# Performance work log

Hardware: AMD Instinct MI355X
Metric: run time of the kernel (lower is better)

## Reference

```python
import jax, jax.numpy as jnp
import numpy as np

B, N, INP = 16, 1024, 256
HEADS, DIM_HEAD = 8, 32
INNER = HEADS * DIM_HEAD  # 256
OUP = 256
IH = IW = 32  # IH*IW == N


def _relative_index(ih, iw):
    # mirrors the torch __init__ construction (meshgrid indexing='ij')
    coords = np.stack(np.meshgrid(np.arange(ih), np.arange(iw), indexing='ij')).reshape(2, -1)
    rel = coords[:, :, None] - coords[:, None, :]  # [2, N, N]
    rel[0] += ih - 1
    rel[1] += iw - 1
    rel[0] *= 2 * iw - 1
    return rel.sum(0).reshape(-1)  # [N*N]


def setup_inputs() -> dict:
    key = jax.random.key(0)
    kx, kqkv, kout, kbias = jax.random.split(key, 4)
    x = jax.random.normal(kx, (B, N, INP), dtype=jnp.float32)
    w_qkv = jax.random.normal(kqkv, (INP, 3 * INNER), dtype=jnp.float32) * 0.02
    w_out = jax.random.normal(kout, (INNER, OUP), dtype=jnp.float32) * 0.02
    b_out = jnp.zeros((OUP,), dtype=jnp.float32)
    bias_table = jax.random.normal(kbias, ((2 * IH - 1) * (2 * IW - 1), HEADS), dtype=jnp.float32) * 0.02
    relative_index = jnp.asarray(_relative_index(IH, IW), dtype=jnp.int32)
    return {"x": x, "w_qkv": w_qkv, "w_out": w_out, "b_out": b_out,
            "bias_table": bias_table, "relative_index": relative_index}


def reference(x, w_qkv, w_out, b_out, bias_table, relative_index):
    b, n, _ = x.shape
    scale = DIM_HEAD ** (-0.5)
    qkv = x @ w_qkv  # [b, n, 3*inner]
    q, k, v = jnp.split(qkv, 3, axis=-1)
    split_heads = lambda t: t.reshape(b, n, HEADS, DIM_HEAD).transpose(0, 2, 1, 3)  # b h n d
    q, k, v = split_heads(q), split_heads(k), split_heads(v)
    dots = jnp.einsum('bhnd,bhmd->bhnm', q, k) * scale  # [b, h, n, n]
    # gather bias: (n*n, heads) -> (1, heads, n, n), matching '(h w) c -> 1 c h w'
    rel_bias = bias_table[relative_index].reshape(n, n, HEADS).transpose(2, 0, 1)[None]
    attn = jax.nn.softmax(dots + rel_bias, axis=-1)
    out = jnp.einsum('bhnm,bhmd->bhnd', attn, v)
    out = out.transpose(0, 2, 1, 3).reshape(b, n, INNER)  # b n (h d)
    return out @ w_out + b_out
```

## Files before the change

### kernel.cpp

```cpp
#include <hip/hip_runtime.h>
#include <hip/hip_bf16.h>

typedef __bf16 bf16;
typedef bf16 bf16x4 __attribute__((ext_vector_type(4)));
typedef bf16 bf16x8 __attribute__((ext_vector_type(8)));
typedef short s16x4 __attribute__((ext_vector_type(4)));
typedef float f32x4 __attribute__((ext_vector_type(4)));

#define MFMA32(A, B, C) __builtin_amdgcn_mfma_f32_16x16x32_bf16(A, B, C, 0, 0, 0)
#define MFMA16(A, B, C) __builtin_amdgcn_mfma_f32_16x16x16bf16_1k(A, B, C, 0, 0, 0)
#define GL2LDS16(gp, lp)                                                            \
  __builtin_amdgcn_global_load_lds((const __attribute__((address_space(1))) unsigned int*)(gp), \
                                   (__attribute__((address_space(3))) unsigned int*)(lp), 16, 0, 0)

static constexpr float SCALE = 0.17677669529663687f;
static constexpr float LOG2E = 1.4426950408889634f;

__global__ __launch_bounds__(256) void k_prep(const float* __restrict__ x,
                                              const float* __restrict__ wqkv,
                                              const float* __restrict__ wout,
                                              const float* __restrict__ table,
                                              const int* __restrict__ ridx,
                                              bf16* __restrict__ xb, bf16* __restrict__ wtq,
                                              bf16* __restrict__ wto, bf16* __restrict__ rbb) {
  const int tid = threadIdx.x;
  const int blk = blockIdx.x;
  if (blk < 2048) {
    int t = blk * 256 + tid;
    const float4* s = reinterpret_cast<const float4*>(x) + (size_t)t * 2;
    float4 a = s[0], c = s[1];
    bf16x8 o;
    o[0] = (bf16)a.x; o[1] = (bf16)a.y; o[2] = (bf16)a.z; o[3] = (bf16)a.w;
    o[4] = (bf16)c.x; o[5] = (bf16)c.y; o[6] = (bf16)c.z; o[7] = (bf16)c.w;
    reinterpret_cast<bf16x8*>(xb)[t] = o;
  } else if (blk < 3072) {
    int t = (blk - 2048) * 256 + tid;
    if (t < 196608) {
      int n = t >> 8, k = t & 255;
      wtq[t] = (bf16)wqkv[k * 768 + n];
    } else {
      int t2 = t - 196608;
      int n = t2 >> 8, k = t2 & 255;
      wto[t2] = (bf16)wout[k * 256 + n];
    }
  } else {
    const int bb2 = blk - 3072;
    const int qt = bb2 >> 6, kt = bb2 & 63;
    const int r = tid & 3, lane = tid >> 2;
    const int ln = lane & 15, quad = lane >> 4;
    const int qrow = qt * 16 + ln;
    const int key = kt * 16 + quad * 4 + r;
    const int idx = ridx[qrow * 1024 + key];
    const float4* p = reinterpret_cast<const float4*>(table) + idx * 2;
    float4 a = p[0], c = p[1];
    float vals[8] = {a.x, a.y, a.z, a.w, c.x, c.y, c.z, c.w};
    const int base = bb2 * 256 + tid;
#pragma unroll
    for (int h = 0; h < 8; ++h) rbb[h * 1048576 + base] = (bf16)(vals[h] * LOG2E);
  }
}

template <int EPI>
__global__ __launch_bounds__(256) void k_gemm(const bf16* __restrict__ A,
                                              const bf16* __restrict__ Bt,
                                              bf16* __restrict__ q, bf16* __restrict__ kk,
                                              bf16* __restrict__ vt, float* __restrict__ out,
                                              const float* __restrict__ bout) {
  __shared__ __align__(16) bf16 As[2][4096];
  __shared__ __align__(16) bf16 Bs[2][4096];
  const int tid = threadIdx.x;
  const int ln = tid & 15, quad = (tid >> 4) & 3, wv = tid >> 6;
  const int wm = (wv >> 1) * 64, wn = (wv & 1) * 64;
  const int m0 = blockIdx.x * 128, n0 = blockIdx.y * 128;
  const int srow = tid >> 2, scg = (tid & 3) * 8;
  const bf16* ag = A + (size_t)(m0 + srow) * 256 + scg;
  const bf16* bg = Bt + (size_t)(n0 + srow) * 256 + scg;
  f32x4 acc[4][4] = {};

  GL2LDS16(ag, &As[0][tid * 8]);
  GL2LDS16(ag + 64 * 256, &As[0][2048 + tid * 8]);
  GL2LDS16(bg, &Bs[0][tid * 8]);
  GL2LDS16(bg + 64 * 256, &Bs[0][2048 + tid * 8]);

#pragma unroll 2
  for (int kt = 0; kt < 256; kt += 32) {
    const int cur = (kt >> 5) & 1, nxt = cur ^ 1;
    __syncthreads();
    if (kt < 224) {
      GL2LDS16(ag + kt + 32, &As[nxt][tid * 8]);
      GL2LDS16(ag + 64 * 256 + kt + 32, &As[nxt][2048 + tid * 8]);
      GL2LDS16(bg + kt + 32, &Bs[nxt][tid * 8]);
      GL2LDS16(bg + 64 * 256 + kt + 32, &Bs[nxt][2048 + tid * 8]);
    }
    bf16x8 af[4], bfr[4];
#pragma unroll
    for (int i = 0; i < 4; ++i)
      af[i] = *reinterpret_cast<const bf16x8*>(&As[cur][(wm + i * 16 + ln) * 32 + quad * 8]);
#pragma unroll
    for (int i = 0; i < 4; ++i)
      bfr[i] = *reinterpret_cast<const bf16x8*>(&Bs[cur][(wn + i * 16 + ln) * 32 + quad * 8]);
#pragma unroll
    for (int i = 0; i < 4; ++i)
#pragma unroll
      for (int j = 0; j < 4; ++j) acc[i][j] = MFMA32(af[i], bfr[j], acc[i][j]);
  }

  if (EPI == 0) {
    const int colbase = n0 + wn;
    const int seg = colbase >> 8;
    const int cb = colbase & 255;
    const float mul = (seg == 0) ? SCALE * LOG2E : 1.0f;
#pragma unroll
    for (int i = 0; i < 4; ++i) {
      const int gm = m0 + wm + i * 16 + quad * 4;
      const int b = gm >> 10;
#pragma unroll
      for (int j = 0; j < 4; ++j) {
        const int gc = cb + j * 16 + ln;
        const int h = gc >> 5, d = gc & 31;
#pragma unroll
        for (int r = 0; r < 4; ++r) {
          const int nseq = (gm + r) & 1023;
          if (seg == 2) {
            vt[(b * 8 + h) * 32768 + d * 1024 + nseq] = (bf16)acc[i][j][r];
          } else {
            bf16* dst = (seg == 0) ? q : kk;
            dst[(b * 8 + h) * 32768 + nseq * 32 + d] = (bf16)(acc[i][j][r] * mul);
          }
        }
      }
    }
  } else {
#pragma unroll
    for (int j = 0; j < 4; ++j) {
      const int gc = n0 + wn + j * 16 + ln;
      const float bb = bout[gc];
#pragma unroll
      for (int i = 0; i < 4; ++i) {
        const int gm = m0 + wm + i * 16 + quad * 4;
#pragma unroll
        for (int r = 0; r < 4; ++r) out[(size_t)(gm + r) * 256 + gc] = acc[i][j][r] + bb;
      }
    }
  }
}

__global__ __launch_bounds__(256, 6) void k_flash(const bf16* __restrict__ qs,
                                                  const bf16* __restrict__ ks,
                                                  const bf16* __restrict__ vtg,
                                                  const bf16* __restrict__ rbb,
                                                  bf16* __restrict__ ao) {
  __shared__ __align__(16) bf16 Ks[2][2048];
  __shared__ __align__(16) bf16 Vs[2][2048];
  const int tid = threadIdx.x;
  const int lane = tid & 63;
  const int ln = lane & 15, quad = lane >> 4, wv = tid >> 6;
  const int blk = blockIdx.x;
  const int bh = blk & 127;
  const int b = bh >> 3, h = bh & 7;
  const int qtw = (blk >> 7) * 4 + wv;
  const int q0 = qtw * 16;
  const bf16* qb = qs + bh * 32768;
  const bf16* kb = ks + bh * 32768;
  const bf16* vb = vtg + bh * 32768;
  const bf16* bbias = rbb + h * 1048576 + qtw * 16384 + lane * 4;

  const bf16* kg = kb + tid * 8;
  const bf16* vg = vb + (tid & 31) * 1024 + (tid >> 5) * 8;

  const bf16x8 qfrag = *reinterpret_cast<const bf16x8*>(&qb[(q0 + ln) * 32 + quad * 8]);

  f32x4 acc0 = {0.f, 0.f, 0.f, 0.f}, acc1 = {0.f, 0.f, 0.f, 0.f};
  float lsum = 0.f;

  bf16x4 cbf[2][4];
#pragma unroll
  for (int nt = 0; nt < 4; ++nt) cbf[0][nt] = *reinterpret_cast<const bf16x4*>(&bbias[nt * 256]);
  GL2LDS16(kg, &Ks[0][tid * 8]);
  GL2LDS16(vg, &Vs[0][tid * 8]);

#pragma unroll 2
  for (int it = 0; it < 16; ++it) {
    const int cur = it & 1, nxt = cur ^ 1;
    const int k0 = it * 64;
    __syncthreads();
    if (it < 15) {
      GL2LDS16(kg + (k0 + 64) * 32, &Ks[nxt][tid * 8]);
      GL2LDS16(vg + k0 + 64, &Vs[nxt][tid * 8]);
#pragma unroll
      for (int nt = 0; nt < 4; ++nt)
        cbf[nxt][nt] = *reinterpret_cast<const bf16x4*>(&bbias[((it + 1) * 4 + nt) * 256]);
    }
    bf16x8 kf[4];
#pragma unroll
    for (int nt = 0; nt < 4; ++nt)
      kf[nt] = *reinterpret_cast<const bf16x8*>(&Ks[cur][(nt * 16 + ln) * 32 + quad * 8]);
    s16x4 vfa[4], vfc[4];
#pragma unroll
    for (int nt = 0; nt < 4; ++nt) {
      const int base = (2 * nt + (quad >> 1)) * 256 + ln * 8 + (quad & 1) * 4;
      vfa[nt] = *reinterpret_cast<const s16x4*>(&Vs[cur][base]);
      vfc[nt] = *reinterpret_cast<const s16x4*>(&Vs[cur][base + 128]);
    }
    f32x4 s[4];
#pragma unroll
    for (int nt = 0; nt < 4; ++nt) {
      f32x4 c;
#pragma unroll
      for (int e = 0; e < 4; ++e) c[e] = (float)cbf[cur][nt][e];
      s[nt] = MFMA32(kf[nt], qfrag, c);
    }
    s16x4 p[4];
#pragma unroll
    for (int nt = 0; nt < 4; ++nt) {
      bf16x4 t;
#pragma unroll
      for (int e = 0; e < 4; ++e) {
        s[nt][e] = __builtin_amdgcn_exp2f(s[nt][e]);
        t[e] = (bf16)s[nt][e];
      }
      lsum += (s[nt][0] + s[nt][1]) + (s[nt][2] + s[nt][3]);
      p[nt] = __builtin_bit_cast(s16x4, t);
    }
    acc0 = MFMA16(p[0], vfa[0], acc0);
    acc1 = MFMA16(p[0], vfc[0], acc1);
    acc0 = MFMA16(p[1], vfa[1], acc0);
    acc1 = MFMA16(p[1], vfc[1], acc1);
    acc0 = MFMA16(p[2], vfa[2], acc0);
    acc1 = MFMA16(p[2], vfc[2], acc1);
    acc0 = MFMA16(p[3], vfa[3], acc0);
    acc1 = MFMA16(p[3], vfc[3], acc1);
  }
  __syncthreads();

  lsum += __shfl_xor(lsum, 16, 64);
  lsum += __shfl_xor(lsum, 32, 64);

#pragma unroll
  for (int r = 0; r < 4; ++r) {
    const float inv = __builtin_amdgcn_rcpf(__shfl(lsum, quad * 4 + r, 64));
    const int row = q0 + quad * 4 + r;
    bf16* po = &ao[(size_t)(b * 1024 + row) * 256 + h * 32 + ln];
    po[0] = (bf16)(acc0[r] * inv);
    po[16] = (bf16)(acc1[r] * inv);
  }
}

extern "C" void kernel_launch(void* const* d_in, const int* in_sizes, int n_in,
                              void* d_out, int out_size, void* d_ws, size_t ws_size,
                              hipStream_t stream) {
  const float* x = (const float*)d_in[0];
  const float* wqkv = (const float*)d_in[1];
  const float* wout = (const float*)d_in[2];
  const float* bout = (const float*)d_in[3];
  const float* btab = (const float*)d_in[4];
  const int* ridx = (const int*)d_in[5];
  float* out = (float*)d_out;

  char* ws = (char*)d_ws;
  bf16* xb  = (bf16*)(ws + 0);
  bf16* wtq = (bf16*)(ws + 8388608);
  bf16* wto = (bf16*)(ws + 8781824);
  bf16* q   = (bf16*)(ws + 8912896);
  bf16* k   = (bf16*)(ws + 17301504);
  bf16* vt  = (bf16*)(ws + 25690112);
  bf16* rb  = (bf16*)(ws + 34078720);
  bf16* ao  = (bf16*)(ws + 50855936);

  k_prep<<<7168, 256, 0, stream>>>(x, wqkv, wout, btab, ridx, xb, wtq, wto, rb);
  k_gemm<0><<<dim3(128, 6), 256, 0, stream>>>(xb, wtq, q, k, vt, nullptr, nullptr);
  k_flash<<<2048, 256, 0, stream>>>(q, k, vt, rb, ao);
  k_gemm<1><<<dim3(128, 2), 256, 0, stream>>>(ao, wto, nullptr, nullptr, nullptr, out, bout);
}
```

Measured before the change: 155.4 us.

## Process two query tiles per wave in flash kernel and vectorize V-transpose stores

New measurement: 163.3 us. +5.1%, slower.

```diff
diff --git a/kernel.cpp b/kernel.cpp
--- a/kernel.cpp
+++ b/kernel.cpp
@@ -109,22 +109,36 @@
     const int colbase = n0 + wn;
     const int seg = colbase >> 8;
     const int cb = colbase & 255;
-    const float mul = (seg == 0) ? SCALE * LOG2E : 1.0f;
-#pragma unroll
-    for (int i = 0; i < 4; ++i) {
-      const int gm = m0 + wm + i * 16 + quad * 4;
-      const int b = gm >> 10;
-#pragma unroll
-      for (int j = 0; j < 4; ++j) {
-        const int gc = cb + j * 16 + ln;
-        const int h = gc >> 5, d = gc & 31;
-#pragma unroll
-        for (int r = 0; r < 4; ++r) {
-          const int nseq = (gm + r) & 1023;
-          if (seg == 2) {
-            vt[(b * 8 + h) * 32768 + d * 1024 + nseq] = (bf16)acc[i][j][r];
-          } else {
-            bf16* dst = (seg == 0) ? q : kk;
+    if (seg == 2) {
+#pragma unroll
+      for (int i = 0; i < 4; ++i) {
+        const int gm = m0 + wm + i * 16 + quad * 4;
+        const int b = gm >> 10;
+        const int nseq = gm & 1023;
+#pragma unroll
+        for (int j = 0; j < 4; ++j) {
+          const int gc = cb + j * 16 + ln;
+          const int h = gc >> 5, d = gc & 31;
+          bf16x4 v4;
+#pragma unroll
+          for (int r = 0; r < 4; ++r) v4[r] = (bf16)acc[i][j][r];
+          *reinterpret_cast<bf16x4*>(&vt[(b * 8 + h) * 32768 + d * 1024 + nseq]) = v4;
+        }
+      }
+    } else {
+      const float mul = (seg == 0) ? SCALE * LOG2E : 1.0f;
+      bf16* dst = (seg == 0) ? q : kk;
+#pragma unroll
+      for (int i = 0; i < 4; ++i) {
+        const int gm = m0 + wm + i * 16 + quad * 4;
+        const int b = gm >> 10;
+#pragma unroll
+        for (int j = 0; j < 4; ++j) {
+          const int gc = cb + j * 16 + ln;
+          const int h = gc >> 5, d = gc & 31;
+#pragma unroll
+          for (int r = 0; r < 4; ++r) {
+            const int nseq = (gm + r) & 1023;
             dst[(b * 8 + h) * 32768 + nseq * 32 + d] = (bf16)(acc[i][j][r] * mul);
           }
         }
@@ -145,7 +159,7 @@
   }
 }
 
-__global__ __launch_bounds__(256, 6) void k_flash(const bf16* __restrict__ qs,
+__global__ __launch_bounds__(256, 4) void k_flash(const bf16* __restrict__ qs,
                                                   const bf16* __restrict__ ks,
                                                   const bf16* __restrict__ vtg,
                                                   const bf16* __restrict__ rbb,
@@ -158,24 +172,30 @@
   const int blk = blockIdx.x;
   const int bh = blk & 127;
   const int b = bh >> 3, h = bh & 7;
-  const int qtw = (blk >> 7) * 4 + wv;
-  const int q0 = qtw * 16;
+  const int tA = (blk >> 7) * 8 + wv * 2;
+  const int tB = tA + 1;
   const bf16* qb = qs + bh * 32768;
   const bf16* kb = ks + bh * 32768;
   const bf16* vb = vtg + bh * 32768;
-  const bf16* bbias = rbb + h * 1048576 + qtw * 16384 + lane * 4;
+  const bf16* bbA = rbb + h * 1048576 + tA * 16384 + lane * 4;
+  const bf16* bbB = rbb + h * 1048576 + tB * 16384 + lane * 4;
 
   const bf16* kg = kb + tid * 8;
   const bf16* vg = vb + (tid & 31) * 1024 + (tid >> 5) * 8;
 
-  const bf16x8 qfrag = *reinterpret_cast<const bf16x8*>(&qb[(q0 + ln) * 32 + quad * 8]);
-
-  f32x4 acc0 = {0.f, 0.f, 0.f, 0.f}, acc1 = {0.f, 0.f, 0.f, 0.f};
-  float lsum = 0.f;
-
-  bf16x4 cbf[2][4];
-#pragma unroll
-  for (int nt = 0; nt < 4; ++nt) cbf[0][nt] = *reinterpret_cast<const bf16x4*>(&bbias[nt * 256]);
+  const bf16x8 qfA = *reinterpret_cast<const bf16x8*>(&qb[(tA * 16 + ln) * 32 + quad * 8]);
+  const bf16x8 qfB = *reinterpret_cast<const bf16x8*>(&qb[(tB * 16 + ln) * 32 + quad * 8]);
+
+  f32x4 accA0 = {0.f, 0.f, 0.f, 0.f}, accA1 = {0.f, 0.f, 0.f, 0.f};
+  f32x4 accB0 = {0.f, 0.f, 0.f, 0.f}, accB1 = {0.f, 0.f, 0.f, 0.f};
+  float lsA = 0.f, lsB = 0.f;
+
+  bf16x4 cbA[2][4], cbB[2][4];
+#pragma unroll
+  for (int nt = 0; nt < 4; ++nt) {
+    cbA[0][nt] = *reinterpret_cast<const bf16x4*>(&bbA[nt * 256]);
+    cbB[0][nt] = *reinterpret_cast<const bf16x4*>(&bbB[nt * 256]);
+  }
   GL2LDS16(kg, &Ks[0][tid * 8]);
   GL2LDS16(vg, &Vs[0][tid * 8]);
 
@@ -188,8 +208,10 @@
       GL2LDS16(kg + (k0 + 64) * 32, &Ks[nxt][tid * 8]);
       GL2LDS16(vg + k0 + 64, &Vs[nxt][tid * 8]);
 #pragma unroll
-      for (int nt = 0; nt < 4; ++nt)
-        cbf[nxt][nt] = *reinterpret_cast<const bf16x4*>(&bbias[((it + 1) * 4 + nt) * 256]);
+      for (int nt = 0; nt < 4; ++nt) {
+        cbA[nxt][nt] = *reinterpret_cast<const bf16x4*>(&bbA[((it + 1) * 4 + nt) * 256]);
+        cbB[nxt][nt] = *reinterpret_cast<const bf16x4*>(&bbB[((it + 1) * 4 + nt) * 256]);
+      }
     }
     bf16x8 kf[4];
 #pragma unroll
@@ -202,47 +224,86 @@
       vfa[nt] = *reinterpret_cast<const s16x4*>(&Vs[cur][base]);
       vfc[nt] = *reinterpret_cast<const s16x4*>(&Vs[cur][base + 128]);
     }
-    f32x4 s[4];
-#pragma unroll
-    for (int nt = 0; nt < 4; ++nt) {
-      f32x4 c;
-#pragma unroll
-      for (int e = 0; e < 4; ++e) c[e] = (float)cbf[cur][nt][e];
-      s[nt] = MFMA32(kf[nt], qfrag, c);
-    }
-    s16x4 p[4];
-#pragma unroll
-    for (int nt = 0; nt < 4; ++nt) {
-      bf16x4 t;
-#pragma unroll
-      for (int e = 0; e < 4; ++e) {
-        s[nt][e] = __builtin_amdgcn_exp2f(s[nt][e]);
-        t[e] = (bf16)s[nt][e];
-      }
-      lsum += (s[nt][0] + s[nt][1]) + (s[nt][2] + s[nt][3]);
-      p[nt] = __builtin_bit_cast(s16x4, t);
-    }
-    acc0 = MFMA16(p[0], vfa[0], acc0);
-    acc1 = MFMA16(p[0], vfc[0], acc1);
-    acc0 = MFMA16(p[1], vfa[1], acc0);
-    acc1 = MFMA16(p[1], vfc[1], acc1);
-    acc0 = MFMA16(p[2], vfa[2], acc0);
-    acc1 = MFMA16(p[2], vfc[2], acc1);
-    acc0 = MFMA16(p[3], vfa[3], acc0);
-    acc1 = MFMA16(p[3], vfc[3], acc1);
+    {
+      f32x4 s[4];
+#pragma unroll
+      for (int nt = 0; nt < 4; ++nt) {
+        f32x4 c;
+#pragma unroll
+        for (int e = 0; e < 4; ++e) c[e] = (float)cbA[cur][nt][e];
+        s[nt] = MFMA32(kf[nt], qfA, c);
+      }
+      s16x4 p[4];
+#pragma unroll
+      for (int nt = 0; nt < 4; ++nt) {
+        bf16x4 t;
+#pragma unroll
+        for (int e = 0; e < 4; ++e) {
+          s[nt][e] = __builtin_amdgcn_exp2f(s[nt][e]);
+          t[e] = (bf16)s[nt][e];
+        }
+        lsA += (s[nt][0] + s[nt][1]) + (s[nt][2] + s[nt][3]);
+        p[nt] = __builtin_bit_cast(s16x4, t);
+      }
+      accA0 = MFMA16(p[0], vfa[0], accA0);
+      accA1 = MFMA16(p[0], vfc[0], accA1);
+      accA0 = MFMA16(p[1], vfa[1], accA0);
+      accA1 = MFMA16(p[1], vfc[1], accA1);
+      accA0 = MFMA16(p[2], vfa[2], accA0);
+      accA1 = MFMA16(p[2], vfc[2], accA1);
+      accA0 = MFMA16(p[3], vfa[3], accA0);
+      accA1 = MFMA16(p[3], vfc[3], accA1);
+    }
+    {
+      f32x4 s[4];
+#pragma unroll
+      for (int nt = 0; nt < 4; ++nt) {
+        f32x4 c;
+#pragma unroll
+        for (int e = 0; e < 4; ++e) c[e] = (float)cbB[cur][nt][e];
+        s[nt] = MFMA32(kf[nt], qfB, c);
+      }
+      s16x4 p[4];
+#pragma unroll
+      for (int nt = 0; nt < 4; ++nt) {
+        bf16x4 t;
+#pragma unroll
+        for (int e = 0; e < 4; ++e) {
+          s[nt][e] = __builtin_amdgcn_exp2f(s[nt][e]);
+          t[e] = (bf16)s[nt][e];
+        }
+        lsB += (s[nt][0] + s[nt][1]) + (s[nt][2] + s[nt][3]);
+        p[nt] = __builtin_bit_cast(s16x4, t);
+      }
+      accB0 = MFMA16(p[0], vfa[0], accB0);
+      accB1 = MFMA16(p[0], vfc[0], accB1);
+      accB0 = MFMA16(p[1], vfa[1], accB0);
+      accB1 = MFMA16(p[1], vfc[1], accB1);
+      accB0 = MFMA16(p[2], vfa[2], accB0);
+      accB1 = MFMA16(p[2], vfc[2], accB1);
+      accB0 = MFMA16(p[3], vfa[3], accB0);
+      accB1 = MFMA16(p[3], vfc[3], accB1);
+    }
   }
   __syncthreads();
 
-  lsum += __shfl_xor(lsum, 16, 64);
-  lsum += __shfl_xor(lsum, 32, 64);
+  lsA += __shfl_xor(lsA, 16, 64);
+  lsA += __shfl_xor(lsA, 32, 64);
+  lsB += __shfl_xor(lsB, 16, 64);
+  lsB += __shfl_xor(lsB, 32, 64);
 
 #pragma unroll
   for (int r = 0; r < 4; ++r) {
-    const float inv = __builtin_amdgcn_rcpf(__shfl(lsum, quad * 4 + r, 64));
-    const int row = q0 + quad * 4 + r;
-    bf16* po = &ao[(size_t)(b * 1024 + row) * 256 + h * 32 + ln];
-    po[0] = (bf16)(acc0[r] * inv);
-    po[16] = (bf16)(acc1[r] * inv);
+    const float invA = __builtin_amdgcn_rcpf(__shfl(lsA, quad * 4 + r, 64));
+    const int rowA = tA * 16 + quad * 4 + r;
+    bf16* poA = &ao[(size_t)(b * 1024 + rowA) * 256 + h * 32 + ln];
+    poA[0] = (bf16)(accA0[r] * invA);
+    poA[16] = (bf16)(accA1[r] * invA);
+    const float invB = __builtin_amdgcn_rcpf(__shfl(lsB, quad * 4 + r, 64));
+    const int rowB = tB * 16 + quad * 4 + r;
+    bf16* poB = &ao[(size_t)(b * 1024 + rowB) * 256 + h * 32 + ln];
+    poB[0] = (bf16)(accB0[r] * invB);
+    poB[16] = (bf16)(accB1[r] * invB);
   }
 }
 
@@ -269,6 +330,6 @@
 
   k_prep<<<7168, 256, 0, stream>>>(x, wqkv, wout, btab, ridx, xb, wtq, wto, rb);
   k_gemm<0><<<dim3(128, 6), 256, 0, stream>>>(xb, wtq, q, k, vt, nullptr, nullptr);
-  k_flash<<<2048, 256, 0, stream>>>(q, k, vt, rb, ao);
+  k_flash<<<1024, 256, 0, stream>>>(q, k, vt, rb, ao);
   k_gemm<1><<<dim3(128, 2), 256, 0, stream>>>(ao, wto, nullptr, nullptr, nullptr, out, bout);
 }
```
